# Optimization experiments

Hardware: AMD Instinct MI355X
Metric: run time of the kernel (lower is better)

## Reference

```python
import jax, jax.numpy as jnp
import numpy as np

N, D, R, T, E = 4096, 1024, 92, 32, 8192
SCALE = float(np.sqrt(2.0 / 7.0))  # matches torch.rand(...) * sqrt(2/7)


def setup_inputs() -> dict:
    key = jax.random.key(0)
    ks = jax.random.split(key, 7)
    x = jax.random.normal(ks[0], (N, D), dtype=jnp.float32)
    edge_tok = jax.random.randint(ks[1], (E,), 0, N)
    edge_rel = jax.random.randint(ks[2], (E,), 0, R)
    W_stack = jax.random.uniform(ks[3], (R, D, D), dtype=jnp.float32) * SCALE  # depWeights
    B_stack = jnp.ones((R, D), dtype=jnp.float32)                              # depBias
    W_self = jax.random.uniform(ks[4], (D, D), dtype=jnp.float32) * SCALE      # self.weight
    b_self = jnp.ones((D,), dtype=jnp.float32)                                 # self.bias
    W_tag = jax.random.normal(ks[5], (D, T), dtype=jnp.float32) * 0.02         # hidden2tag
    b_tag = jnp.zeros((T,), dtype=jnp.float32)
    return {"x": x, "W_self": W_self, "b_self": b_self, "W_stack": W_stack,
            "B_stack": B_stack, "W_tag": W_tag, "b_tag": b_tag,
            "edge_tok": edge_tok, "edge_rel": edge_rel}


def reference(x, W_self, b_self, W_stack, B_stack, W_tag, b_tag, edge_tok, edge_rel):
    n, r = x.shape[0], W_stack.shape[0]
    # C[i, r] = number of dependency edges of token i with relation r
    C = jnp.zeros((n, r), dtype=x.dtype).at[edge_tok, edge_rel].add(jnp.asarray(1.0, x.dtype))
    self_out = x @ W_self + b_self  # [N, D]
    # accum_i = self_out_i + sum_{dep in deps(i)} (x_i @ W_dep + b_dep)
    #         = self_out_i + sum_r C[i, r] * (x_i @ W_r) + (C @ B_stack)_i
    def body(acc, wc):
        Wr, Cr = wc  # Wr: [D, D], Cr: [N]
        return acc + Cr[:, None] * (x @ Wr), None
    dep_out, _ = jax.lax.scan(body, jnp.zeros_like(self_out), (W_stack, C.T))
    h = jax.nn.relu(self_out + dep_out + C @ B_stack)  # [N, D]
    tag_scores = jax.nn.log_softmax(h @ W_tag + b_tag, axis=1)  # [N, T]
    return tag_scores, h
```

## Files before the change

kernel.cpp:

```cpp
#include <hip/hip_runtime.h>
#include <hip/hip_bf16.h>
#include <math.h>

#define N_TOK 4096
#define D_DIM 1024
#define R_REL 92
#define T_TAG 32
#define E_EDGE 8192
#define SELF_R 127
#define GRID_ITEMS 192


typedef short bf16x8 __attribute__((ext_vector_type(8)));
typedef float f32x4 __attribute__((ext_vector_type(4)));

union Pk8 { uint4 q; unsigned short s[8]; };
union Pk4 { uint2 d; unsigned short s[4]; };

__device__ __forceinline__ unsigned short f2bf(float f) {
    union { __hip_bfloat16 b; unsigned short u; } c;
    c.b = __float2bfloat16(f);
    return c.u;
}

__global__ __launch_bounds__(1024) void k_setup(const int* __restrict__ rel,
                                                const int* __restrict__ tokv,
                                                int* __restrict__ ws) {
    __shared__ int cnt[128], offL[128], cur[128];
    __shared__ int sh[1024];
    __shared__ int tcnt[4096], toff[4096];
    int t = threadIdx.x;
    if (t < 128) { cnt[t] = 0; cur[t] = 0; }
    #pragma unroll
    for (int i = 0; i < 4; ++i) tcnt[i * 1024 + t] = 0;
    __syncthreads();
    int er[8], et[8];
    #pragma unroll
    for (int i = 0; i < 8; ++i) {
        er[i] = rel[i * 1024 + t];
        et[i] = tokv[i * 1024 + t];
        atomicAdd(&cnt[er[i]], 1);
        atomicAdd(&tcnt[et[i]], 1);
    }
    __syncthreads();
    int c = (t < 128) ? cnt[t] : 0;
    int v = c;
    if (t < 128) sh[t] = v;
    __syncthreads();
    for (int st = 1; st < 128; st <<= 1) {
        int add = (t >= st && t < 128) ? sh[t - st] : 0;
        __syncthreads();
        if (t < 128) { v += add; sh[t] = v; }
        __syncthreads();
    }
    if (t < 128) { offL[t] = v - c; ws[256 + t] = v - c; ws[t] = c; }
    int ch = (t < R_REL) ? ((c + 127) >> 7) : 0;
    int v2 = ch;
    if (t < 128) sh[t] = v2;
    __syncthreads();
    for (int st = 1; st < 128; st <<= 1) {
        int add = (t >= st && t < 128) ? sh[t - st] : 0;
        __syncthreads();
        if (t < 128) { v2 += add; sh[t] = v2; }
        __syncthreads();
    }
    if (t < 32) ws[512 + t] = (SELF_R << 16) | t;
    if (t < R_REL) {
        int excl = v2 - ch;
        for (int j = 0; j < ch; ++j)
            ws[512 + 32 + excl + j] = (t << 16) | j;
    }
    if (t == 127) ws[384] = 32 + v2;
    int s0 = tcnt[4 * t + 0], s1 = tcnt[4 * t + 1];
    int s2 = tcnt[4 * t + 2], s3 = tcnt[4 * t + 3];
    int sum4 = s0 + s1 + s2 + s3;
    int vv = sum4;
    sh[t] = vv;
    __syncthreads();
    for (int st = 1; st < 1024; st <<= 1) {
        int add = (t >= st) ? sh[t - st] : 0;
        __syncthreads();
        vv += add; sh[t] = vv;
        __syncthreads();
    }
    int ex = vv - sum4;
    toff[4 * t + 0] = ex;
    toff[4 * t + 1] = ex + s0;
    toff[4 * t + 2] = ex + s0 + s1;
    toff[4 * t + 3] = ex + s0 + s1 + s2;
    ws[17408 + 4 * t + 0] = toff[4 * t + 0];
    ws[17408 + 4 * t + 1] = toff[4 * t + 1];
    ws[17408 + 4 * t + 2] = toff[4 * t + 2];
    ws[17408 + 4 * t + 3] = toff[4 * t + 3];
    if (t == 1023) ws[17408 + 4096] = vv;
    __syncthreads();
    #pragma unroll
    for (int i = 0; i < 4; ++i) tcnt[i * 1024 + t] = 0;
    __syncthreads();
    #pragma unroll
    for (int i = 0; i < 8; ++i) {
        int pos = offL[er[i]] + atomicAdd(&cur[er[i]], 1);
        ws[1024 + pos] = et[i];
        int q = toff[et[i]] + atomicAdd(&tcnt[et[i]], 1);
        ws[22528 + q] = pos;
    }
}

__global__ __launch_bounds__(256, 2) void k_fused(const float* __restrict__ x,
                                                  const float* __restrict__ Wself,
                                                  const float* __restrict__ bself,
                                                  const float* __restrict__ Wst,
                                                  const float* __restrict__ Bst,
                                                  const int* __restrict__ ws,
                                                  float* __restrict__ scratch) {
    if ((int)blockIdx.x >= ws[384]) return;
    int item = ws[512 + blockIdx.x];
    int r = item >> 16, chunk = item & 0xFFFF;
    int m0 = chunk * 128;
    int valid;
    const float* Wbase;
    const float* bias;
    bool is_self = (r == SELF_R);
    int off0 = 0;
    if (is_self) {
        valid = 128;
        Wbase = Wself;
        bias = bself;
    } else {
        int cnt = ws[r];
        off0 = ws[256 + r];
        valid = cnt - m0; if (valid > 128) valid = 128;
        Wbase = Wst + (size_t)r * D_DIM * D_DIM;
        bias = Bst + (size_t)r * D_DIM;
    }
    int srow_base = is_self ? (8192 + m0) : (off0 + m0);

    __shared__ unsigned short Al[128 * 64];
    __shared__ unsigned short Bl[128 * 64];
    __shared__ int toks[128];
    char* Alb = (char*)Al;
    char* Blb = (char*)Bl;
    int t = threadIdx.x;
    if (t < 128) {
        int tok;
        if (is_self) tok = m0 + t;
        else tok = (t < valid) ? ws[1024 + off0 + m0 + t] : 0;
        toks[t] = tok;
    }
    __syncthreads();

    int gn0 = blockIdx.y * 128;
    int w = t >> 6, l = t & 63;
    int lr = l & 15, lg = l >> 4;
    int wm = (w >> 1) * 64, wn = (w & 1) * 64;
    int ar = t >> 4, ac = t & 15;
    int tok_s[8];
    #pragma unroll
    for (int s = 0; s < 8; ++s) tok_s[s] = toks[s * 16 + ar];
    int bn = (w & 1) * 64 + l;
    int bkb = (w >> 1) * 32;
    const float* wcol = Wbase + gn0 + bn;

    float4 pa[8];
    float pb[32];

    #pragma unroll
    for (int s = 0; s < 8; ++s)
        pa[s] = *(const float4*)(x + (size_t)tok_s[s] * D_DIM + ac * 4);
    #pragma unroll
    for (int s = 0; s < 4; ++s)
        #pragma unroll
        for (int i = 0; i < 8; ++i)
            pb[s * 8 + i] = wcol[(size_t)(bkb + s * 8 + i) * D_DIM];
    #pragma unroll
    for (int s = 0; s < 8; ++s) {
        int row = s * 16 + ar;
        Pk4 u;
        u.s[0] = f2bf(pa[s].x); u.s[1] = f2bf(pa[s].y);
        u.s[2] = f2bf(pa[s].z); u.s[3] = f2bf(pa[s].w);
        *(uint2*)(Alb + row * 128 + ((ac * 8) ^ ((row & 7) << 4))) = u.d;
    }
    #pragma unroll
    for (int s = 0; s < 4; ++s) {
        Pk8 u;
        #pragma unroll
        for (int i = 0; i < 8; ++i) u.s[i] = f2bf(pb[s * 8 + i]);
        *(uint4*)(Blb + bn * 128 + ((bkb * 2 + s * 16) ^ ((bn & 7) << 4))) = u.q;
    }
    __syncthreads();

    f32x4 acc[4][4] = {};
    for (int k0 = 0; k0 < D_DIM; k0 += 64) {
        bool pf = (k0 + 64 < D_DIM);
        if (pf) {
            int kn = k0 + 64;
            #pragma unroll
            for (int s = 0; s < 8; ++s)
                pa[s] = *(const float4*)(x + (size_t)tok_s[s] * D_DIM + kn + ac * 4);
            #pragma unroll
            for (int s = 0; s < 4; ++s)
                #pragma unroll
                for (int i = 0; i < 8; ++i)
                    pb[s * 8 + i] = wcol[(size_t)(kn + bkb + s * 8 + i) * D_DIM];
        }
        #pragma unroll
        for (int kk = 0; kk < 2; ++kk) {
            int koff = kk * 64 + lg * 16;
            bf16x8 af[4], bfr[4];
            #pragma unroll
            for (int mi = 0; mi < 4; ++mi)
                af[mi] = *(const bf16x8*)(Alb + (wm + mi * 16 + lr) * 128 +
                                          (koff ^ ((lr & 7) << 4)));
            #pragma unroll
            for (int ni = 0; ni < 4; ++ni)
                bfr[ni] = *(const bf16x8*)(Blb + (wn + ni * 16 + lr) * 128 +
                                           (koff ^ ((lr & 7) << 4)));
            #pragma unroll
            for (int mi = 0; mi < 4; ++mi)
                #pragma unroll
                for (int ni = 0; ni < 4; ++ni)
                    acc[mi][ni] = __builtin_amdgcn_mfma_f32_16x16x32_bf16(
                        af[mi], bfr[ni], acc[mi][ni], 0, 0, 0);
        }
        __syncthreads();
        if (pf) {
            #pragma unroll
            for (int s = 0; s < 8; ++s) {
                int row = s * 16 + ar;
                Pk4 u;
                u.s[0] = f2bf(pa[s].x); u.s[1] = f2bf(pa[s].y);
                u.s[2] = f2bf(pa[s].z); u.s[3] = f2bf(pa[s].w);
                *(uint2*)(Alb + row * 128 + ((ac * 8) ^ ((row & 7) << 4))) = u.d;
            }
            #pragma unroll
            for (int s = 0; s < 4; ++s) {
                Pk8 u;
                #pragma unroll
                for (int i = 0; i < 8; ++i) u.s[i] = f2bf(pb[s * 8 + i]);
                *(uint4*)(Blb + bn * 128 + ((bkb * 2 + s * 16) ^ ((bn & 7) << 4))) = u.q;
            }
            __syncthreads();
        }
    }
    float bb[4];
    #pragma unroll
    for (int ni = 0; ni < 4; ++ni) bb[ni] = bias[gn0 + wn + ni * 16 + lr];
    #pragma unroll
    for (int mi = 0; mi < 4; ++mi)
        #pragma unroll
        for (int j = 0; j < 4; ++j) {
            int rl = wm + mi * 16 + lg * 4 + j;
            if (rl < valid) {
                float* dst = scratch + (size_t)(srow_base + rl) * D_DIM + gn0 + wn + lr;
                #pragma unroll
                for (int ni = 0; ni < 4; ++ni)
                    dst[ni * 16] = acc[mi][ni][j] + bb[ni];
            }
        }
}

__global__ __launch_bounds__(256) void k_reduce(const int* __restrict__ ws,
                                                const float* __restrict__ scratch,
                                                float* __restrict__ out_h) {
    int tok = blockIdx.x;
    int t = threadIdx.x;
    int j0 = ws[17408 + tok], j1 = ws[17408 + tok + 1];
    float4 a = *(const float4*)(scratch + (size_t)(8192 + tok) * D_DIM + t * 4);
    for (int j = j0; j < j1; ++j) {
        int p = ws[22528 + j];
        float4 d = *(const float4*)(scratch + (size_t)p * D_DIM + t * 4);
        a.x += d.x; a.y += d.y; a.z += d.z; a.w += d.w;
    }
    a.x = fmaxf(a.x, 0.f); a.y = fmaxf(a.y, 0.f);
    a.z = fmaxf(a.z, 0.f); a.w = fmaxf(a.w, 0.f);
    *(float4*)(out_h + (size_t)tok * D_DIM + t * 4) = a;
}

__global__ __launch_bounds__(256) void k_tag(const float* __restrict__ out_h,
                                             const float* __restrict__ Wt,
                                             const float* __restrict__ bt,
                                             float* __restrict__ out_tag) {
    __shared__ unsigned short Al[64 * 64];
    __shared__ unsigned short Bl[32 * 64];
    char* Alb = (char*)Al;
    char* Blb = (char*)Bl;
    int tok0 = blockIdx.x * 64;
    int t = threadIdx.x;
    int w = t >> 6, l = t & 63, lr = l & 15, lg = l >> 4;
    int wm = w * 16;
    int ar = t >> 4, ac = t & 15;
    int bn = t & 31, kh = t >> 5;
    f32x4 acc[2] = {};
    for (int k0 = 0; k0 < D_DIM; k0 += 64) {
        __syncthreads();
        #pragma unroll
        for (int s = 0; s < 4; ++s) {
            int row = s * 16 + ar;
            const float* hp = out_h + (size_t)(tok0 + row) * D_DIM + k0 + ac * 4;
            float4 v = *(const float4*)hp;
            Pk4 u;
            u.s[0] = f2bf(v.x); u.s[1] = f2bf(v.y);
            u.s[2] = f2bf(v.z); u.s[3] = f2bf(v.w);
            *(uint2*)(Alb + row * 128 + ((ac * 8) ^ ((row & 7) << 4))) = u.d;
        }
        {
            Pk8 u;
            #pragma unroll
            for (int i = 0; i < 8; ++i)
                u.s[i] = f2bf(Wt[(size_t)(k0 + kh * 8 + i) * T_TAG + bn]);
            *(uint4*)(Blb + bn * 128 + ((kh * 16) ^ ((bn & 7) << 4))) = u.q;
        }
        __syncthreads();
        #pragma unroll
        for (int kk = 0; kk < 2; ++kk) {
            int koff = kk * 64 + lg * 16;
            bf16x8 af = *(const bf16x8*)(Alb + (wm + lr) * 128 +
                                         (koff ^ ((lr & 7) << 4)));
            #pragma unroll
            for (int ni = 0; ni < 2; ++ni) {
                bf16x8 bfr = *(const bf16x8*)(Blb + (ni * 16 + lr) * 128 +
                                              (koff ^ ((lr & 7) << 4)));
                acc[ni] = __builtin_amdgcn_mfma_f32_16x16x32_bf16(
                    af, bfr, acc[ni], 0, 0, 0);
            }
        }
    }
    float bt0 = bt[lr], bt1 = bt[16 + lr];
    #pragma unroll
    for (int j = 0; j < 4; ++j) {
        float v0 = acc[0][j] + bt0;
        float v1 = acc[1][j] + bt1;
        float m = fmaxf(v0, v1);
        #pragma unroll
        for (int s = 1; s < 16; s <<= 1) m = fmaxf(m, __shfl_xor(m, s));
        float sum = expf(v0 - m) + expf(v1 - m);
        #pragma unroll
        for (int s = 1; s < 16; s <<= 1) sum += __shfl_xor(sum, s);
        float lse = m + logf(sum);
        int row = tok0 + wm + lg * 4 + j;
        out_tag[(size_t)row * T_TAG + lr] = v0 - lse;
        out_tag[(size_t)row * T_TAG + 16 + lr] = v1 - lse;
    }
}

extern "C" void kernel_launch(void* const* d_in, const int* in_sizes, int n_in,
                              void* d_out, int out_size, void* d_ws, size_t ws_size,
                              hipStream_t stream) {
    const float* x     = (const float*)d_in[0];
    const float* Wself = (const float*)d_in[1];
    const float* bself = (const float*)d_in[2];
    const float* Wst   = (const float*)d_in[3];
    const float* Bst   = (const float*)d_in[4];
    const float* Wtag  = (const float*)d_in[5];
    const float* btag  = (const float*)d_in[6];
    const int*   etok  = (const int*)d_in[7];
    const int*   erel  = (const int*)d_in[8];
    float* out_tag = (float*)d_out;
    float* out_h   = (float*)d_out + (size_t)N_TOK * T_TAG;
    int* ws = (int*)d_ws;
    float* scratch = (float*)d_ws + 32768;

    k_setup<<<1, 1024, 0, stream>>>(erel, etok, ws);
    k_fused<<<dim3(GRID_ITEMS, D_DIM / 128), 256, 0, stream>>>(
        x, Wself, bself, Wst, Bst, ws, scratch);
    k_reduce<<<N_TOK, 256, 0, stream>>>(ws, scratch, out_h);
    k_tag<<<N_TOK / 64, 256, 0, stream>>>(out_h, Wtag, btag, out_tag);
}
```

Before: 158.2 us.

## Store GEMM scratch in bf16, double-buffer LDS tiles, warp-shuffle token scan

Three separate changes. The per-relation GEMM results are written to scratch as bf16 instead of fp32, which halves the scratch write and reduce-read traffic; the reduction widens them back to fp32. The fused GEMM's LDS tiles are double-buffered so one of the two barriers per k-step goes away. The setup kernel's 1024-wide token prefix scan becomes a wavefront shuffle scan plus a small cross-wave scan. Rounding the intermediates to bf16 before summation adds some accuracy error, and doubling LDS to 64KB per block may lower occupancy.

```diff
diff --git a/kernel.cpp b/kernel.cpp
--- a/kernel.cpp
+++ b/kernel.cpp
@@ -22,14 +22,19 @@
     c.b = __float2bfloat16(f);
     return c.u;
 }
+__device__ __forceinline__ float bf2f(unsigned short u) {
+    return __uint_as_float(((unsigned)u) << 16);
+}
 
 __global__ __launch_bounds__(1024) void k_setup(const int* __restrict__ rel,
                                                 const int* __restrict__ tokv,
                                                 int* __restrict__ ws) {
     __shared__ int cnt[128], offL[128], cur[128];
-    __shared__ int sh[1024];
+    __shared__ int sh[128];
+    __shared__ int wsum[16];
     __shared__ int tcnt[4096], toff[4096];
     int t = threadIdx.x;
+    int lane = t & 63, wid = t >> 6;
     if (t < 128) { cnt[t] = 0; cur[t] = 0; }
     #pragma unroll
     for (int i = 0; i < 4; ++i) tcnt[i * 1024 + t] = 0;
@@ -75,24 +80,35 @@
     int s2 = tcnt[4 * t + 2], s3 = tcnt[4 * t + 3];
     int sum4 = s0 + s1 + s2 + s3;
     int vv = sum4;
-    sh[t] = vv;
-    __syncthreads();
-    for (int st = 1; st < 1024; st <<= 1) {
-        int add = (t >= st) ? sh[t - st] : 0;
-        __syncthreads();
-        vv += add; sh[t] = vv;
-        __syncthreads();
-    }
-    int ex = vv - sum4;
+    #pragma unroll
+    for (int d = 1; d < 64; d <<= 1) {
+        int n = __shfl_up(vv, d);
+        if (lane >= d) vv += n;
+    }
+    if (lane == 63) wsum[wid] = vv;
+    __syncthreads();
+    if (wid == 0) {
+        int wv = (lane < 16) ? wsum[lane] : 0;
+        #pragma unroll
+        for (int d = 1; d < 16; d <<= 1) {
+            int n = __shfl_up(wv, d);
+            if (lane >= d) wv += n;
+        }
+        if (lane < 16) wsum[lane] = wv;
+    }
+    __syncthreads();
+    int base = (wid > 0) ? wsum[wid - 1] : 0;
+    int incl = base + vv;
+    int ex = incl - sum4;
     toff[4 * t + 0] = ex;
     toff[4 * t + 1] = ex + s0;
     toff[4 * t + 2] = ex + s0 + s1;
     toff[4 * t + 3] = ex + s0 + s1 + s2;
-    ws[17408 + 4 * t + 0] = toff[4 * t + 0];
-    ws[17408 + 4 * t + 1] = toff[4 * t + 1];
-    ws[17408 + 4 * t + 2] = toff[4 * t + 2];
-    ws[17408 + 4 * t + 3] = toff[4 * t + 3];
-    if (t == 1023) ws[17408 + 4096] = vv;
+    ws[17408 + 4 * t + 0] = ex;
+    ws[17408 + 4 * t + 1] = ex + s0;
+    ws[17408 + 4 * t + 2] = ex + s0 + s1;
+    ws[17408 + 4 * t + 3] = ex + s0 + s1 + s2;
+    if (t == 1023) ws[17408 + 4096] = incl;
     __syncthreads();
     #pragma unroll
     for (int i = 0; i < 4; ++i) tcnt[i * 1024 + t] = 0;
@@ -112,7 +128,7 @@
                                                   const float* __restrict__ Wst,
                                                   const float* __restrict__ Bst,
                                                   const int* __restrict__ ws,
-                                                  float* __restrict__ scratch) {
+                                                  unsigned short* __restrict__ scratch) {
     if ((int)blockIdx.x >= ws[384]) return;
     int item = ws[512 + blockIdx.x];
     int r = item >> 16, chunk = item & 0xFFFF;
@@ -135,11 +151,9 @@
     }
     int srow_base = is_self ? (8192 + m0) : (off0 + m0);
 
-    __shared__ unsigned short Al[128 * 64];
-    __shared__ unsigned short Bl[128 * 64];
+    __shared__ unsigned short Al[2][128 * 64];
+    __shared__ unsigned short Bl[2][128 * 64];
     __shared__ int toks[128];
-    char* Alb = (char*)Al;
-    char* Blb = (char*)Bl;
     int t = threadIdx.x;
     if (t < 128) {
         int tok;
@@ -172,24 +186,29 @@
         #pragma unroll
         for (int i = 0; i < 8; ++i)
             pb[s * 8 + i] = wcol[(size_t)(bkb + s * 8 + i) * D_DIM];
-    #pragma unroll
-    for (int s = 0; s < 8; ++s) {
-        int row = s * 16 + ar;
-        Pk4 u;
-        u.s[0] = f2bf(pa[s].x); u.s[1] = f2bf(pa[s].y);
-        u.s[2] = f2bf(pa[s].z); u.s[3] = f2bf(pa[s].w);
-        *(uint2*)(Alb + row * 128 + ((ac * 8) ^ ((row & 7) << 4))) = u.d;
-    }
-    #pragma unroll
-    for (int s = 0; s < 4; ++s) {
-        Pk8 u;
-        #pragma unroll
-        for (int i = 0; i < 8; ++i) u.s[i] = f2bf(pb[s * 8 + i]);
-        *(uint4*)(Blb + bn * 128 + ((bkb * 2 + s * 16) ^ ((bn & 7) << 4))) = u.q;
+    {
+        char* Ab = (char*)Al[0];
+        char* Bb = (char*)Bl[0];
+        #pragma unroll
+        for (int s = 0; s < 8; ++s) {
+            int row = s * 16 + ar;
+            Pk4 u;
+            u.s[0] = f2bf(pa[s].x); u.s[1] = f2bf(pa[s].y);
+            u.s[2] = f2bf(pa[s].z); u.s[3] = f2bf(pa[s].w);
+            *(uint2*)(Ab + row * 128 + ((ac * 8) ^ ((row & 7) << 4))) = u.d;
+        }
+        #pragma unroll
+        for (int s = 0; s < 4; ++s) {
+            Pk8 u;
+            #pragma unroll
+            for (int i = 0; i < 8; ++i) u.s[i] = f2bf(pb[s * 8 + i]);
+            *(uint4*)(Bb + bn * 128 + ((bkb * 2 + s * 16) ^ ((bn & 7) << 4))) = u.q;
+        }
     }
     __syncthreads();
 
     f32x4 acc[4][4] = {};
+    int cur = 0;
     for (int k0 = 0; k0 < D_DIM; k0 += 64) {
         bool pf = (k0 + 64 < D_DIM);
         if (pf) {
@@ -203,17 +222,19 @@
                 for (int i = 0; i < 8; ++i)
                     pb[s * 8 + i] = wcol[(size_t)(kn + bkb + s * 8 + i) * D_DIM];
         }
+        char* Ac = (char*)Al[cur];
+        char* Bc = (char*)Bl[cur];
         #pragma unroll
         for (int kk = 0; kk < 2; ++kk) {
             int koff = kk * 64 + lg * 16;
             bf16x8 af[4], bfr[4];
             #pragma unroll
             for (int mi = 0; mi < 4; ++mi)
-                af[mi] = *(const bf16x8*)(Alb + (wm + mi * 16 + lr) * 128 +
+                af[mi] = *(const bf16x8*)(Ac + (wm + mi * 16 + lr) * 128 +
                                           (koff ^ ((lr & 7) << 4)));
             #pragma unroll
             for (int ni = 0; ni < 4; ++ni)
-                bfr[ni] = *(const bf16x8*)(Blb + (wn + ni * 16 + lr) * 128 +
+                bfr[ni] = *(const bf16x8*)(Bc + (wn + ni * 16 + lr) * 128 +
                                            (koff ^ ((lr & 7) << 4)));
             #pragma unroll
             for (int mi = 0; mi < 4; ++mi)
@@ -222,25 +243,27 @@
                     acc[mi][ni] = __builtin_amdgcn_mfma_f32_16x16x32_bf16(
                         af[mi], bfr[ni], acc[mi][ni], 0, 0, 0);
         }
-        __syncthreads();
         if (pf) {
+            char* An = (char*)Al[cur ^ 1];
+            char* Bn = (char*)Bl[cur ^ 1];
             #pragma unroll
             for (int s = 0; s < 8; ++s) {
                 int row = s * 16 + ar;
                 Pk4 u;
                 u.s[0] = f2bf(pa[s].x); u.s[1] = f2bf(pa[s].y);
                 u.s[2] = f2bf(pa[s].z); u.s[3] = f2bf(pa[s].w);
-                *(uint2*)(Alb + row * 128 + ((ac * 8) ^ ((row & 7) << 4))) = u.d;
+                *(uint2*)(An + row * 128 + ((ac * 8) ^ ((row & 7) << 4))) = u.d;
             }
             #pragma unroll
             for (int s = 0; s < 4; ++s) {
                 Pk8 u;
                 #pragma unroll
                 for (int i = 0; i < 8; ++i) u.s[i] = f2bf(pb[s * 8 + i]);
-                *(uint4*)(Blb + bn * 128 + ((bkb * 2 + s * 16) ^ ((bn & 7) << 4))) = u.q;
+                *(uint4*)(Bn + bn * 128 + ((bkb * 2 + s * 16) ^ ((bn & 7) << 4))) = u.q;
             }
-            __syncthreads();
-        }
+        }
+        __syncthreads();
+        cur ^= 1;
     }
     float bb[4];
     #pragma unroll
@@ -251,29 +274,32 @@
         for (int j = 0; j < 4; ++j) {
             int rl = wm + mi * 16 + lg * 4 + j;
             if (rl < valid) {
-                float* dst = scratch + (size_t)(srow_base + rl) * D_DIM + gn0 + wn + lr;
+                unsigned short* dst = scratch +
+                    (size_t)(srow_base + rl) * D_DIM + gn0 + wn + lr;
                 #pragma unroll
                 for (int ni = 0; ni < 4; ++ni)
-                    dst[ni * 16] = acc[mi][ni][j] + bb[ni];
+                    dst[ni * 16] = f2bf(acc[mi][ni][j] + bb[ni]);
             }
         }
 }
 
 __global__ __launch_bounds__(256) void k_reduce(const int* __restrict__ ws,
-                                                const float* __restrict__ scratch,
+                                                const unsigned short* __restrict__ scratch,
                                                 float* __restrict__ out_h) {
     int tok = blockIdx.x;
     int t = threadIdx.x;
     int j0 = ws[17408 + tok], j1 = ws[17408 + tok + 1];
-    float4 a = *(const float4*)(scratch + (size_t)(8192 + tok) * D_DIM + t * 4);
+    ushort4 sv = *(const ushort4*)(scratch + (size_t)(8192 + tok) * D_DIM + t * 4);
+    float a0 = bf2f(sv.x), a1 = bf2f(sv.y), a2 = bf2f(sv.z), a3 = bf2f(sv.w);
     for (int j = j0; j < j1; ++j) {
         int p = ws[22528 + j];
-        float4 d = *(const float4*)(scratch + (size_t)p * D_DIM + t * 4);
-        a.x += d.x; a.y += d.y; a.z += d.z; a.w += d.w;
-    }
-    a.x = fmaxf(a.x, 0.f); a.y = fmaxf(a.y, 0.f);
-    a.z = fmaxf(a.z, 0.f); a.w = fmaxf(a.w, 0.f);
-    *(float4*)(out_h + (size_t)tok * D_DIM + t * 4) = a;
+        ushort4 dv = *(const ushort4*)(scratch + (size_t)p * D_DIM + t * 4);
+        a0 += bf2f(dv.x); a1 += bf2f(dv.y); a2 += bf2f(dv.z); a3 += bf2f(dv.w);
+    }
+    float4 o;
+    o.x = fmaxf(a0, 0.f); o.y = fmaxf(a1, 0.f);
+    o.z = fmaxf(a2, 0.f); o.w = fmaxf(a3, 0.f);
+    *(float4*)(out_h + (size_t)tok * D_DIM + t * 4) = o;
 }
 
 __global__ __launch_bounds__(256) void k_tag(const float* __restrict__ out_h,
@@ -358,7 +384,7 @@
     float* out_tag = (float*)d_out;
     float* out_h   = (float*)d_out + (size_t)N_TOK * T_TAG;
     int* ws = (int*)d_ws;
-    float* scratch = (float*)d_ws + 32768;
+    unsigned short* scratch = (unsigned short*)((int*)d_ws + 32768);
 
     k_setup<<<1, 1024, 0, stream>>>(erel, etok, ws);
     k_fused<<<dim3(GRID_ITEMS, D_DIM / 128), 256, 0, stream>>>(
```

New measurement: 149.4 us. 1.06x faster.
